# Optimization experiments

Measured on AMD Instinct MI355X. Metric: run time of the kernel, lower is better.

The kernel has to match this reference:

```python
import jax, jax.numpy as jnp
import numpy as np

N_NODES = 100000
N_EDGES = 1600000
D_IN = 64
D_OUT = 64


def setup_inputs() -> dict:
    key = jax.random.key(0)
    k_x, k_e, k_wl, k_bl, k_wr = jax.random.split(key, 5)
    x = jax.random.normal(k_x, (N_NODES, D_IN), dtype=jnp.float32)
    edge_index = jax.random.randint(k_e, (2, N_EDGES), 0, N_NODES, dtype=jnp.int64)
    W_l = jax.random.normal(k_wl, (D_IN, D_OUT), dtype=jnp.float32) / np.sqrt(D_IN)
    b_l = jax.random.normal(k_bl, (D_OUT,), dtype=jnp.float32) * 0.01
    W_r = jax.random.normal(k_wr, (D_IN, D_OUT), dtype=jnp.float32) / np.sqrt(D_IN)
    return {"x": x, "edge_index": edge_index, "W_l": W_l, "b_l": b_l, "W_r": W_r}


def reference(x, edge_index, W_l, b_l, W_r):
    # SAGEConv (mean aggregation) + ReLU:
    #   out_i = relu( W_l^T mean_{j->i} x_j + b_l + W_r^T x_i )
    n = x.shape[0]
    src, dst = edge_index[0], edge_index[1]
    # gather source features and mean-aggregate into destination nodes
    agg = jax.ops.segment_sum(x[src], dst, num_segments=n)           # [N, D_IN]
    cnt = jax.ops.segment_sum(jnp.ones_like(dst, dtype=x.dtype), dst, num_segments=n)
    mean_nbr = agg / jnp.maximum(cnt, 1.0)[:, None]                   # [N, D_IN]
    out = mean_nbr @ W_l + b_l + x @ W_r                              # [N, D_OUT]
    return jax.nn.relu(out)
```

## Files before the change

### kernel.cpp

```cpp
#include <hip/hip_runtime.h>

#define N_NODES 100000
#define N_EDGES 1600000
#define D 64
#define NBKT 391
#define REG 5120
#define A_EPB 4096
#define SCB 1024
#define A_I4 (A_EPB / 4)
#define N_I4 (N_EDGES / 4)
#define TB 5

typedef __attribute__((ext_vector_type(8))) short bf16x8;
typedef __attribute__((ext_vector_type(4))) float f32x4;

__device__ __forceinline__ unsigned short f2bf(float f) {
    union { float f; unsigned u; } v; v.f = f;
    unsigned r = v.u + 0x7FFFu + ((v.u >> 16) & 1u);
    return (unsigned short)(r >> 16);
}

#define CVT_ITEMS ((N_NODES * D) / 4)
#define CVT_BLKS 1563
__global__ __launch_bounds__(SCB) void scatter_cvt(const float* __restrict__ x,
                                                   unsigned* __restrict__ xq,
                                                   const int* __restrict__ ei,
                                                   unsigned* __restrict__ fc,
                                                   unsigned* __restrict__ bpairs) {
    __shared__ unsigned hc[NBKT];
    __shared__ unsigned hb[NBKT];
    const int blk = blockIdx.x;
    const int tid = threadIdx.x;
    if (blk < NBKT) {
        if (tid < NBKT) hc[tid] = 0;
        __syncthreads();

        const int g = blk * A_I4 + tid;
        const int4* sptr = (const int4*)ei;
        const int4* dptr = (const int4*)(ei + N_EDGES);

        unsigned pay[4];
        unsigned meta[4];
        if (g < N_I4) {
            int4 s4 = sptr[g];
            int4 d4 = dptr[g];
            const int dd[4] = { d4.x, d4.y, d4.z, d4.w };
            const int ss[4] = { s4.x, s4.y, s4.z, s4.w };
            #pragma unroll
            for (int c = 0; c < 4; ++c) {
                const unsigned b = (unsigned)dd[c] >> 8;
                const unsigned lr = atomicAdd(&hc[b], 1u);
                meta[c] = (b << 13) | lr;
                pay[c]  = ((unsigned)ss[c] << 8) | ((unsigned)dd[c] & 255u);
            }
        } else {
            #pragma unroll
            for (int c = 0; c < 4; ++c) meta[c] = 0xFFFFFFFFu;
        }
        __syncthreads();
        if (tid < NBKT) {
            unsigned c = hc[tid];
            if (c) hb[tid] = atomicAdd(&fc[tid], c);
        }
        __syncthreads();
        #pragma unroll
        for (int e = 0; e < 4; ++e) {
            if (meta[e] != 0xFFFFFFFFu) {
                const unsigned b   = meta[e] >> 13;
                const unsigned lr  = meta[e] & 0x1FFFu;
                const unsigned pos = hb[b] + lr;
                if (pos < REG) bpairs[(size_t)b * REG + pos] = pay[e];
            }
        }
    } else {
        const int j = (blk - NBKT) * SCB + tid;
        if (j < CVT_ITEMS) {
            float4 v = ((const float4*)x)[j];
            unsigned u = __builtin_amdgcn_cvt_pk_fp8_f32(v.x, v.y, 0u, false);
            u = __builtin_amdgcn_cvt_pk_fp8_f32(v.z, v.w, u, true);
            xq[j] = u;
        }
    }
}

__global__ __launch_bounds__(SCB) void bucket_csr(const unsigned* __restrict__ fc,
                                                  unsigned* __restrict__ bpairs,
                                                  int* __restrict__ offsets) {
    __shared__ unsigned ncnt[256];
    __shared__ unsigned s[256];
    const int b   = blockIdx.x;
    const int tid = threadIdx.x;
    const unsigned base = (unsigned)b * REG;
    unsigned cnt = fc[b];
    if (cnt > REG) cnt = REG;

    if (tid < 256) ncnt[tid] = 0;
    __syncthreads();

    unsigned pk[TB];
    unsigned rk[TB];
    #pragma unroll
    for (int t = 0; t < TB; ++t) {
        const unsigned i = (unsigned)tid + t * (unsigned)SCB;
        if (i < cnt) {
            const unsigned p = bpairs[base + i];
            pk[t] = p;
            rk[t] = atomicAdd(&ncnt[p & 255u], 1u);
        } else {
            pk[t] = 0xFFFFFFFFu;
        }
    }
    __syncthreads();

    unsigned v = 0;
    if (tid < 256) { v = ncnt[tid]; s[tid] = v; }
    __syncthreads();
    for (int off = 1; off < 256; off <<= 1) {
        unsigned u = 0;
        if (tid < 256 && tid >= off) u = s[tid - off];
        __syncthreads();
        if (tid < 256) s[tid] += u;
        __syncthreads();
    }
    if (tid < 256) {
        const unsigned excl = s[tid] - v;
        ncnt[tid] = excl;
        const int n0 = b * 256;
        if (n0 + tid < N_NODES) offsets[n0 + tid] = (int)((v << 13) | excl);
    }
    __syncthreads();

    #pragma unroll
    for (int t = 0; t < TB; ++t) {
        if (pk[t] != 0xFFFFFFFFu) {
            const unsigned p  = pk[t];
            const unsigned dl = p & 255u;
            bpairs[base + ncnt[dl] + rk[t]] = p >> 8;
        }
    }
}

#define STEPF(SI, J, N, A0, A1, A2, A3)                                      \
    {                                                                         \
        _Pragma("unroll")                                                     \
        for (int t_ = 0; t_ < 4; ++t_) {                                      \
            const int e_  = (J) + 4 * t_;                                     \
            const int sel_ = __shfl((SI), e_ + grp, 64);                      \
            unsigned v_ = xq32[(size_t)sel_ * 16 + lq];                       \
            v_ = (e_ + grp < (N)) ? v_ : 0u;                                  \
            (A0) += __builtin_amdgcn_cvt_f32_fp8(v_, 0);                      \
            (A1) += __builtin_amdgcn_cvt_f32_fp8(v_, 1);                      \
            (A2) += __builtin_amdgcn_cvt_f32_fp8(v_, 2);                      \
            (A3) += __builtin_amdgcn_cvt_f32_fp8(v_, 3);                      \
        }                                                                     \
    }

#define TAILF(S0, DD, A0, A1, A2, A3)                                        \
    for (int b2_ = 64; b2_ < (DD); b2_ += 64) {                              \
        const int n2_ = ((DD) - b2_ < 64) ? ((DD) - b2_) : 64;               \
        const int cl2_ = (lane < n2_) ? lane : (n2_ - 1);                    \
        const int sit_ = csr[(S0) + b2_ + cl2_];                             \
        for (int j_ = 0; j_ < n2_; j_ += 16) {                               \
            STEPF(sit_, j_, n2_, A0, A1, A2, A3)                             \
        }                                                                     \
    }

#define FINR(R, DV, A0, A1, A2, A3)                                          \
    {                                                                         \
        (A0) += __shfl_xor((A0), 16, 64); (A0) += __shfl_xor((A0), 32, 64);   \
        (A1) += __shfl_xor((A1), 16, 64); (A1) += __shfl_xor((A1), 32, 64);   \
        (A2) += __shfl_xor((A2), 16, 64); (A2) += __shfl_xor((A2), 32, 64);   \
        (A3) += __shfl_xor((A3), 16, 64); (A3) += __shfl_xor((A3), 32, 64);   \
        const float inv_ = 1.0f / fmaxf((float)(DV), 1.0f);                   \
        if (lane < 16) {                                                      \
            const unsigned m0_ = ((unsigned)f2bf((A1) * inv_) << 16)          \
                                 | f2bf((A0) * inv_);                         \
            const unsigned m1_ = ((unsigned)f2bf((A3) * inv_) << 16)          \
                                 | f2bf((A2) * inv_);                         \
            const int sw_ = ((R) & 7) << 2;                                   \
            sAw[((R) * 64 + 2 * lane) ^ sw_]     = m0_;                       \
            sAw[((R) * 64 + 2 * lane + 1) ^ sw_] = m1_;                       \
        }                                                                     \
    }

#define NPW 16
#define SBLK 512
__global__ __launch_bounds__(SBLK) void sage_kernel(const float* __restrict__ x,
                                                    const unsigned* __restrict__ xq32,
                                                    const int* __restrict__ offsets,
                                                    const int* __restrict__ csr,
                                                    const float* __restrict__ Wl,
                                                    const float* __restrict__ bl,
                                                    const float* __restrict__ Wr,
                                                    float* __restrict__ out) {
    __shared__ unsigned short sWt[D * 2 * D];
    __shared__ float sbl[D];
    __shared__ unsigned int sA32[(SBLK / 64) * NPW * (2 * D / 2)];

    const int tid = threadIdx.x;
    for (int i = tid; i < D * D; i += SBLK) {
        int k = i >> 6, c = i & 63;
        int swz = (c & 7) << 3;
        sWt[(c * 128 + k) ^ swz]      = f2bf(Wl[i]);
        sWt[(c * 128 + 64 + k) ^ swz] = f2bf(Wr[i]);
    }
    if (tid < D) sbl[tid] = bl[tid];
    __syncthreads();

    const int lane = tid & 63;
    const int wib  = tid >> 6;
    const int wid  = (blockIdx.x * (SBLK / 64)) + wib;
    const int node0 = wid * NPW;
    if (node0 >= N_NODES) return;

    unsigned int* sAw = sA32 + wib * (NPW * 64);
    const int grp = lane >> 4;
    const int lq  = lane & 15;
    const int bb = (node0 >> 8) * REG;

    {
        const float2* __restrict__ x2 = (const float2*)x;
        const int c = lane & 31;
        #pragma unroll
        for (int rr = 0; rr < 8; ++rr) {
            const int r = 2 * rr + (lane >> 5);
            float2 v = x2[(size_t)(node0 + r) * 32 + c];
            const unsigned mp = ((unsigned)f2bf(v.y) << 16) | f2bf(v.x);
            sAw[(r * 64 + 32 + c) ^ ((r & 7) << 2)] = mp;
        }
    }

    const int offl = offsets[node0 + (lane & 15)];

    int si[NPW];
    int dg[NPW];
    #pragma unroll
    for (int r = 0; r < NPW; ++r) {
        const int er = __builtin_amdgcn_readlane(offl, r);
        const int d  = (int)((unsigned)er >> 13);
        dg[r] = d;
        const int s0 = bb + (er & 0x1FFF);
        const int dm = (d > 0) ? d : 1;
        const int cl = (lane < dm) ? lane : (dm - 1);
        si[r] = csr[s0 + cl];
    }

    #pragma unroll
    for (int p = 0; p < NPW / 2; ++p) {
        const int rA = 2 * p, rB = 2 * p + 1;
        const int dA = dg[rA], dB = dg[rB];
        const int nA = (dA < 64) ? dA : 64;
        const int nB = (dB < 64) ? dB : 64;

        float a0 = 0.0f, a1 = 0.0f, a2 = 0.0f, a3 = 0.0f;
        float b0 = 0.0f, b1 = 0.0f, b2 = 0.0f, b3 = 0.0f;
        int jA = 0, jB = 0;
        while (jA < nA && jB < nB) {
            STEPF(si[rA], jA, nA, a0, a1, a2, a3)
            STEPF(si[rB], jB, nB, b0, b1, b2, b3)
            jA += 16; jB += 16;
        }
        while (jA < nA) { STEPF(si[rA], jA, nA, a0, a1, a2, a3) jA += 16; }
        while (jB < nB) { STEPF(si[rB], jB, nB, b0, b1, b2, b3) jB += 16; }
        if (dA > 64) {
            const int s0A = bb + (__builtin_amdgcn_readlane(offl, rA) & 0x1FFF);
            TAILF(s0A, dA, a0, a1, a2, a3)
        }
        if (dB > 64) {
            const int s0B = bb + (__builtin_amdgcn_readlane(offl, rB) & 0x1FFF);
            TAILF(s0B, dB, b0, b1, b2, b3)
        }

        FINR(rA, dA, a0, a1, a2, a3)
        FINR(rB, dB, b0, b1, b2, b3)
    }

    const unsigned short* sAu = (const unsigned short*)sAw;
    const int row = lane & 15;
    const int kb  = lane >> 4;

    bf16x8 afr[4];
    #pragma unroll
    for (int kc = 0; kc < 4; ++kc) {
        int us = (row * 128 + kc * 32 + kb * 8) ^ ((row & 7) << 3);
        afr[kc] = *(const bf16x8*)(sAu + us);
    }

    #pragma unroll
    for (int ct = 0; ct < 4; ++ct) {
        const int col = ct * 16 + row;
        f32x4 acc = {0.0f, 0.0f, 0.0f, 0.0f};
        #pragma unroll
        for (int kc = 0; kc < 4; ++kc) {
            int us = (col * 128 + kc * 32 + kb * 8) ^ ((col & 7) << 3);
            bf16x8 bfr = *(const bf16x8*)(sWt + us);
            acc = __builtin_amdgcn_mfma_f32_16x16x32_bf16(afr[kc], bfr, acc, 0, 0, 0);
        }
        const float bias = sbl[col];
        const int crow0 = (lane >> 4) * 4;
        #pragma unroll
        for (int i = 0; i < 4; ++i) {
            out[(node0 + crow0 + i) * D + col] = fmaxf(acc[i] + bias, 0.0f);
        }
    }
}

extern "C" void kernel_launch(void* const* d_in, const int* in_sizes, int n_in,
                              void* d_out, int out_size, void* d_ws, size_t ws_size,
                              hipStream_t stream) {
    const float* x  = (const float*)d_in[0];
    const int*   ei = (const int*)d_in[1];
    const float* Wl = (const float*)d_in[2];
    const float* bl = (const float*)d_in[3];
    const float* Wr = (const float*)d_in[4];
    float* out = (float*)d_out;

    unsigned* xq      = (unsigned*)d_ws;
    unsigned* fc      = xq + (size_t)N_NODES * 16;
    int* offsets      = (int*)(fc + 512);
    unsigned* bpairs  = (unsigned*)(offsets + 100004);

    hipMemsetAsync(fc, 0, 512 * sizeof(unsigned), stream);

    scatter_cvt<<<NBKT + CVT_BLKS, SCB, 0, stream>>>(x, xq, ei, fc, bpairs);
    bucket_csr<<<NBKT, SCB, 0, stream>>>(fc, bpairs, offsets);

    {
        const int waves  = (N_NODES + NPW - 1) / NPW;
        const int blocks = (waves + (SBLK / 64) - 1) / (SBLK / 64);
        sage_kernel<<<blocks, SBLK, 0, stream>>>(x, xq, offsets, (const int*)bpairs,
                                                 Wl, bl, Wr, out);
    }
}
```

Baseline: 84.77 us.

## Fuse bucket CSR construction into the SAGE kernel using shared memory

Drops the separate bucket_csr launch and builds each bucket's local CSR (per-node degrees, offsets and sorted source indices) in LDS inside sage_kernel. Each 512-thread block now handles one 256-node bucket, and each wave processes two 16-node groups. This removes a kernel launch and the global round trip for offsets and the sorted CSR. The cost is far fewer blocks (391 instead of about 782), more LDS per block, and a serial counting-sort phase before the gather, all of which can hurt occupancy and latency hiding.

```diff
diff --git a/kernel.cpp b/kernel.cpp
--- a/kernel.cpp
+++ b/kernel.cpp
@@ -5,11 +5,10 @@
 #define D 64
 #define NBKT 391
 #define REG 5120
-#define A_EPB 4096
 #define SCB 1024
-#define A_I4 (A_EPB / 4)
+#define A_I4 1024
 #define N_I4 (N_EDGES / 4)
-#define TB 5
+#define TBC 10
 
 typedef __attribute__((ext_vector_type(8))) short bf16x8;
 typedef __attribute__((ext_vector_type(4))) float f32x4;
@@ -83,63 +82,6 @@
     }
 }
 
-__global__ __launch_bounds__(SCB) void bucket_csr(const unsigned* __restrict__ fc,
-                                                  unsigned* __restrict__ bpairs,
-                                                  int* __restrict__ offsets) {
-    __shared__ unsigned ncnt[256];
-    __shared__ unsigned s[256];
-    const int b   = blockIdx.x;
-    const int tid = threadIdx.x;
-    const unsigned base = (unsigned)b * REG;
-    unsigned cnt = fc[b];
-    if (cnt > REG) cnt = REG;
-
-    if (tid < 256) ncnt[tid] = 0;
-    __syncthreads();
-
-    unsigned pk[TB];
-    unsigned rk[TB];
-    #pragma unroll
-    for (int t = 0; t < TB; ++t) {
-        const unsigned i = (unsigned)tid + t * (unsigned)SCB;
-        if (i < cnt) {
-            const unsigned p = bpairs[base + i];
-            pk[t] = p;
-            rk[t] = atomicAdd(&ncnt[p & 255u], 1u);
-        } else {
-            pk[t] = 0xFFFFFFFFu;
-        }
-    }
-    __syncthreads();
-
-    unsigned v = 0;
-    if (tid < 256) { v = ncnt[tid]; s[tid] = v; }
-    __syncthreads();
-    for (int off = 1; off < 256; off <<= 1) {
-        unsigned u = 0;
-        if (tid < 256 && tid >= off) u = s[tid - off];
-        __syncthreads();
-        if (tid < 256) s[tid] += u;
-        __syncthreads();
-    }
-    if (tid < 256) {
-        const unsigned excl = s[tid] - v;
-        ncnt[tid] = excl;
-        const int n0 = b * 256;
-        if (n0 + tid < N_NODES) offsets[n0 + tid] = (int)((v << 13) | excl);
-    }
-    __syncthreads();
-
-    #pragma unroll
-    for (int t = 0; t < TB; ++t) {
-        if (pk[t] != 0xFFFFFFFFu) {
-            const unsigned p  = pk[t];
-            const unsigned dl = p & 255u;
-            bpairs[base + ncnt[dl] + rk[t]] = p >> 8;
-        }
-    }
-}
-
 #define STEPF(SI, J, N, A0, A1, A2, A3)                                      \
     {                                                                         \
         _Pragma("unroll")                                                     \
@@ -159,7 +101,7 @@
     for (int b2_ = 64; b2_ < (DD); b2_ += 64) {                              \
         const int n2_ = ((DD) - b2_ < 64) ? ((DD) - b2_) : 64;               \
         const int cl2_ = (lane < n2_) ? lane : (n2_ - 1);                    \
-        const int sit_ = csr[(S0) + b2_ + cl2_];                             \
+        const int sit_ = csrL[(S0) + b2_ + cl2_];                            \
         for (int j_ = 0; j_ < n2_; j_ += 16) {                               \
             STEPF(sit_, j_, n2_, A0, A1, A2, A3)                             \
         }                                                                     \
@@ -183,21 +125,26 @@
         }                                                                     \
     }
 
-#define NPW 16
 #define SBLK 512
 __global__ __launch_bounds__(SBLK) void sage_kernel(const float* __restrict__ x,
                                                     const unsigned* __restrict__ xq32,
-                                                    const int* __restrict__ offsets,
-                                                    const int* __restrict__ csr,
+                                                    const unsigned* __restrict__ fc,
+                                                    const unsigned* __restrict__ bpairs,
                                                     const float* __restrict__ Wl,
                                                     const float* __restrict__ bl,
                                                     const float* __restrict__ Wr,
                                                     float* __restrict__ out) {
     __shared__ unsigned short sWt[D * 2 * D];
     __shared__ float sbl[D];
-    __shared__ unsigned int sA32[(SBLK / 64) * NPW * (2 * D / 2)];
-
+    __shared__ int csrL[REG];
+    __shared__ unsigned sdeg[256];
+    __shared__ unsigned soff[256];
+    __shared__ unsigned sscan[256];
+    __shared__ unsigned sA32[(SBLK / 64) * 16 * 64];
+
+    const int b   = blockIdx.x;
     const int tid = threadIdx.x;
+
     for (int i = tid; i < D * D; i += SBLK) {
         int k = i >> 6, c = i & 63;
         int swz = (c & 7) << 3;
@@ -205,102 +152,143 @@
         sWt[(c * 128 + 64 + k) ^ swz] = f2bf(Wr[i]);
     }
     if (tid < D) sbl[tid] = bl[tid];
+    if (tid < 256) sdeg[tid] = 0;
+    __syncthreads();
+
+    unsigned cnt = fc[b];
+    if (cnt > REG) cnt = REG;
+    unsigned pk[TBC];
+    unsigned rk[TBC];
+    #pragma unroll
+    for (int t = 0; t < TBC; ++t) {
+        const unsigned i = (unsigned)tid + t * (unsigned)SBLK;
+        if (i < cnt) {
+            const unsigned p = bpairs[(size_t)b * REG + i];
+            pk[t] = p;
+            rk[t] = atomicAdd(&sdeg[p & 255u], 1u);
+        } else {
+            pk[t] = 0xFFFFFFFFu;
+        }
+    }
+    __syncthreads();
+    unsigned v = 0;
+    if (tid < 256) { v = sdeg[tid]; sscan[tid] = v; }
+    __syncthreads();
+    for (int off = 1; off < 256; off <<= 1) {
+        unsigned u = 0;
+        if (tid < 256 && tid >= off) u = sscan[tid - off];
+        __syncthreads();
+        if (tid < 256) sscan[tid] += u;
+        __syncthreads();
+    }
+    if (tid < 256) soff[tid] = sscan[tid] - v;
+    __syncthreads();
+    #pragma unroll
+    for (int t = 0; t < TBC; ++t) {
+        if (pk[t] != 0xFFFFFFFFu) {
+            const unsigned p  = pk[t];
+            const unsigned dl = p & 255u;
+            csrL[soff[dl] + rk[t]] = (int)(p >> 8);
+        }
+    }
     __syncthreads();
 
     const int lane = tid & 63;
     const int wib  = tid >> 6;
-    const int wid  = (blockIdx.x * (SBLK / 64)) + wib;
-    const int node0 = wid * NPW;
-    if (node0 >= N_NODES) return;
-
-    unsigned int* sAw = sA32 + wib * (NPW * 64);
+    unsigned int* sAw = sA32 + wib * (16 * 64);
     const int grp = lane >> 4;
     const int lq  = lane & 15;
-    const int bb = (node0 >> 8) * REG;
-
-    {
-        const float2* __restrict__ x2 = (const float2*)x;
-        const int c = lane & 31;
-        #pragma unroll
-        for (int rr = 0; rr < 8; ++rr) {
-            const int r = 2 * rr + (lane >> 5);
-            float2 v = x2[(size_t)(node0 + r) * 32 + c];
-            const unsigned mp = ((unsigned)f2bf(v.y) << 16) | f2bf(v.x);
-            sAw[(r * 64 + 32 + c) ^ ((r & 7) << 2)] = mp;
-        }
-    }
-
-    const int offl = offsets[node0 + (lane & 15)];
-
-    int si[NPW];
-    int dg[NPW];
-    #pragma unroll
-    for (int r = 0; r < NPW; ++r) {
-        const int er = __builtin_amdgcn_readlane(offl, r);
-        const int d  = (int)((unsigned)er >> 13);
-        dg[r] = d;
-        const int s0 = bb + (er & 0x1FFF);
-        const int dm = (d > 0) ? d : 1;
-        const int cl = (lane < dm) ? lane : (dm - 1);
-        si[r] = csr[s0 + cl];
-    }
-
-    #pragma unroll
-    for (int p = 0; p < NPW / 2; ++p) {
-        const int rA = 2 * p, rB = 2 * p + 1;
-        const int dA = dg[rA], dB = dg[rB];
-        const int nA = (dA < 64) ? dA : 64;
-        const int nB = (dB < 64) ? dB : 64;
-
-        float a0 = 0.0f, a1 = 0.0f, a2 = 0.0f, a3 = 0.0f;
-        float b0 = 0.0f, b1 = 0.0f, b2 = 0.0f, b3 = 0.0f;
-        int jA = 0, jB = 0;
-        while (jA < nA && jB < nB) {
-            STEPF(si[rA], jA, nA, a0, a1, a2, a3)
-            STEPF(si[rB], jB, nB, b0, b1, b2, b3)
-            jA += 16; jB += 16;
-        }
-        while (jA < nA) { STEPF(si[rA], jA, nA, a0, a1, a2, a3) jA += 16; }
-        while (jB < nB) { STEPF(si[rB], jB, nB, b0, b1, b2, b3) jB += 16; }
-        if (dA > 64) {
-            const int s0A = bb + (__builtin_amdgcn_readlane(offl, rA) & 0x1FFF);
-            TAILF(s0A, dA, a0, a1, a2, a3)
-        }
-        if (dB > 64) {
-            const int s0B = bb + (__builtin_amdgcn_readlane(offl, rB) & 0x1FFF);
-            TAILF(s0B, dB, b0, b1, b2, b3)
-        }
-
-        FINR(rA, dA, a0, a1, a2, a3)
-        FINR(rB, dB, b0, b1, b2, b3)
-    }
-
-    const unsigned short* sAu = (const unsigned short*)sAw;
-    const int row = lane & 15;
-    const int kb  = lane >> 4;
-
-    bf16x8 afr[4];
-    #pragma unroll
-    for (int kc = 0; kc < 4; ++kc) {
-        int us = (row * 128 + kc * 32 + kb * 8) ^ ((row & 7) << 3);
-        afr[kc] = *(const bf16x8*)(sAu + us);
-    }
-
-    #pragma unroll
-    for (int ct = 0; ct < 4; ++ct) {
-        const int col = ct * 16 + row;
-        f32x4 acc = {0.0f, 0.0f, 0.0f, 0.0f};
+
+    for (int h = 0; h < 2; ++h) {
+        const int loc0  = wib * 32 + h * 16;
+        const int node0 = b * 256 + loc0;
+        if (node0 >= N_NODES) break;
+
+        {
+            const float2* __restrict__ x2 = (const float2*)x;
+            const int c = lane & 31;
+            #pragma unroll
+            for (int rr = 0; rr < 8; ++rr) {
+                const int r = 2 * rr + (lane >> 5);
+                float2 vv = x2[(size_t)(node0 + r) * 32 + c];
+                const unsigned mp = ((unsigned)f2bf(vv.y) << 16) | f2bf(vv.x);
+                sAw[(r * 64 + 32 + c) ^ ((r & 7) << 2)] = mp;
+            }
+        }
+
+        const int l16  = lane & 15;
+        const int offl = (int)((sdeg[loc0 + l16] << 13) | soff[loc0 + l16]);
+
+        int si[16];
+        int dg[16];
+        #pragma unroll
+        for (int r = 0; r < 16; ++r) {
+            const int er = __builtin_amdgcn_readlane(offl, r);
+            const int d  = (int)((unsigned)er >> 13);
+            dg[r] = d;
+            const int s0 = er & 0x1FFF;
+            const int dm = (d > 0) ? d : 1;
+            const int cl = (lane < dm) ? lane : (dm - 1);
+            si[r] = csrL[s0 + cl];
+        }
+
+        #pragma unroll
+        for (int p = 0; p < 8; ++p) {
+            const int rA = 2 * p, rB = 2 * p + 1;
+            const int dA = dg[rA], dB = dg[rB];
+            const int nA = (dA < 64) ? dA : 64;
+            const int nB = (dB < 64) ? dB : 64;
+
+            float a0 = 0.0f, a1 = 0.0f, a2 = 0.0f, a3 = 0.0f;
+            float b0 = 0.0f, b1 = 0.0f, b2 = 0.0f, b3 = 0.0f;
+            int jA = 0, jB = 0;
+            while (jA < nA && jB < nB) {
+                STEPF(si[rA], jA, nA, a0, a1, a2, a3)
+                STEPF(si[rB], jB, nB, b0, b1, b2, b3)
+                jA += 16; jB += 16;
+            }
+            while (jA < nA) { STEPF(si[rA], jA, nA, a0, a1, a2, a3) jA += 16; }
+            while (jB < nB) { STEPF(si[rB], jB, nB, b0, b1, b2, b3) jB += 16; }
+            if (dA > 64) {
+                const int s0A = __builtin_amdgcn_readlane(offl, rA) & 0x1FFF;
+                TAILF(s0A, dA, a0, a1, a2, a3)
+            }
+            if (dB > 64) {
+                const int s0B = __builtin_amdgcn_readlane(offl, rB) & 0x1FFF;
+                TAILF(s0B, dB, b0, b1, b2, b3)
+            }
+
+            FINR(rA, dA, a0, a1, a2, a3)
+            FINR(rB, dB, b0, b1, b2, b3)
+        }
+
+        const unsigned short* sAu = (const unsigned short*)sAw;
+        const int row = lane & 15;
+        const int kb  = lane >> 4;
+
+        bf16x8 afr[4];
         #pragma unroll
         for (int kc = 0; kc < 4; ++kc) {
-            int us = (col * 128 + kc * 32 + kb * 8) ^ ((col & 7) << 3);
-            bf16x8 bfr = *(const bf16x8*)(sWt + us);
-            acc = __builtin_amdgcn_mfma_f32_16x16x32_bf16(afr[kc], bfr, acc, 0, 0, 0);
-        }
-        const float bias = sbl[col];
-        const int crow0 = (lane >> 4) * 4;
-        #pragma unroll
-        for (int i = 0; i < 4; ++i) {
-            out[(node0 + crow0 + i) * D + col] = fmaxf(acc[i] + bias, 0.0f);
+            int us = (row * 128 + kc * 32 + kb * 8) ^ ((row & 7) << 3);
+            afr[kc] = *(const bf16x8*)(sAu + us);
+        }
+
+        #pragma unroll
+        for (int ct = 0; ct < 4; ++ct) {
+            const int col = ct * 16 + row;
+            f32x4 acc = {0.0f, 0.0f, 0.0f, 0.0f};
+            #pragma unroll
+            for (int kc = 0; kc < 4; ++kc) {
+                int us = (col * 128 + kc * 32 + kb * 8) ^ ((col & 7) << 3);
+                bf16x8 bfr = *(const bf16x8*)(sWt + us);
+                acc = __builtin_amdgcn_mfma_f32_16x16x32_bf16(afr[kc], bfr, acc, 0, 0, 0);
+            }
+            const float bias = sbl[col];
+            const int crow0 = (lane >> 4) * 4;
+            #pragma unroll
+            for (int i = 0; i < 4; ++i) {
+                out[(node0 + crow0 + i) * D + col] = fmaxf(acc[i] + bias, 0.0f);
+            }
         }
     }
 }
@@ -317,18 +305,11 @@
 
     unsigned* xq      = (unsigned*)d_ws;
     unsigned* fc      = xq + (size_t)N_NODES * 16;
-    int* offsets      = (int*)(fc + 512);
-    unsigned* bpairs  = (unsigned*)(offsets + 100004);
+    unsigned* bpairs  = fc + 512;
 
     hipMemsetAsync(fc, 0, 512 * sizeof(unsigned), stream);
 
     scatter_cvt<<<NBKT + CVT_BLKS, SCB, 0, stream>>>(x, xq, ei, fc, bpairs);
-    bucket_csr<<<NBKT, SCB, 0, stream>>>(fc, bpairs, offsets);
-
-    {
-        const int waves  = (N_NODES + NPW - 1) / NPW;
-        const int blocks = (waves + (SBLK / 64) - 1) / (SBLK / 64);
-        sage_kernel<<<blocks, SBLK, 0, stream>>>(x, xq, offsets, (const int*)bpairs,
-                                                 Wl, bl, Wr, out);
-    }
+
+    sage_kernel<<<NBKT, SBLK, 0, stream>>>(x, xq, fc, bpairs, Wl, bl, Wr, out);
 }
```

After: 77.51 us. 1.09x faster.
